# Kernel tuning notes

Measured on AMD Instinct MI355X. Metric: run time of the kernel, lower is better.

The kernel has to match this reference:

```python
import jax, jax.numpy as jnp
import numpy as np

B = 2
L = 1024
D_MODEL = 1024
D_INNER = 2048   # expand * d_model
D_STATE = 16
DT_RANK = 64     # ceil(d_model / 16)
D_CONV = 4


def setup_inputs() -> dict:
    key = jax.random.key(0)
    ks = jax.random.split(key, 8)
    def nrm(k, shape, scale):
        return jax.random.normal(k, shape, dtype=jnp.float32) * scale
    A_log = jnp.log(jnp.tile(jnp.arange(1, D_STATE + 1, dtype=jnp.float32)[None, :], (D_INNER, 1)))
    return dict(
        hidden_states=jax.random.normal(ks[0], (B, L, D_MODEL), dtype=jnp.float32),
        Win=nrm(ks[1], (D_MODEL, 2 * D_INNER), D_MODEL ** -0.5),
        Wx=nrm(ks[2], (D_INNER, DT_RANK + 2 * D_STATE), D_INNER ** -0.5),
        Wdt=nrm(ks[3], (DT_RANK, D_INNER), DT_RANK ** -0.5),
        dt_bias=nrm(ks[4], (D_INNER,), 1.0),
        Wout=nrm(ks[5], (D_INNER, D_MODEL), D_INNER ** -0.5),
        dw_kernel=nrm(ks[6], (D_CONV, D_INNER), 0.2),
        dw_bias=jnp.zeros((D_INNER,), dtype=jnp.float32),
        A_log=A_log,
        Dskip=jnp.ones((D_INNER,), dtype=jnp.float32),
    )


def _causal_depthwise_conv(x, kernel, bias):
    # x: (B, L, D_INNER), kernel: (k, D_INNER); dilation 1, causal left pad
    k = kernel.shape[0]
    Lq = x.shape[1]
    xpad = jnp.pad(x, ((0, 0), (k - 1, 0), (0, 0)))
    y = sum(xpad[:, i:i + Lq, :] * kernel[i] for i in range(k)) + bias
    return jax.nn.silu(y)


def _selective_scan(u, delta, A, Bm, Cm, Dskip, z):
    # u, delta, z: (B, L, D); A: (D, N); Bm, Cm: (B, L, N)
    deltaA = jnp.exp(jnp.einsum('bld,dn->bldn', delta, A))      # (B,L,D,N)
    deltaBu = jnp.einsum('bld,bln,bld->bldn', delta, Bm, u)     # (B,L,D,N)

    def step(x_prev, elems):
        dA, dBu, c = elems                                      # (B,D,N),(B,D,N),(B,N)
        x_new = dA * x_prev + dBu
        y = jnp.einsum('bdn,bn->bd', x_new, c)
        return x_new, y

    x0 = jnp.zeros((u.shape[0], u.shape[2], A.shape[1]), dtype=jnp.float32)
    _, ys = jax.lax.scan(
        step, x0,
        (deltaA.transpose(1, 0, 2, 3), deltaBu.transpose(1, 0, 2, 3), Cm.transpose(1, 0, 2)))
    y = ys.transpose(1, 0, 2) + u * Dskip                        # skip connection
    return y * jax.nn.silu(z)


def reference(hidden_states, Win, Wx, Wdt, dt_bias, Wout, dw_kernel, dw_bias, A_log, Dskip):
    xz = hidden_states @ Win                                     # (B,L,2*D_INNER)
    x, z = jnp.split(xz, 2, axis=-1)
    A = -jnp.exp(A_log)                                          # (D_INNER, D_STATE)
    x = _causal_depthwise_conv(x, dw_kernel, dw_bias)
    x_dbl = x @ Wx                                               # (B,L,DT_RANK+2*N)
    dt, Bm, Cm = jnp.split(x_dbl, [DT_RANK, DT_RANK + D_STATE], axis=-1)
    delta = jax.nn.softplus(dt @ Wdt + dt_bias)                  # delta_bias + softplus
    y = _selective_scan(x, delta, A, Bm, Cm, Dskip, z)
    return y @ Wout
```

## Files before the change

kernel.cpp:

```cpp
#include <hip/hip_runtime.h>
#include <hip/hip_bf16.h>
#include <math.h>

#define B_SZ 2
#define L_SZ 1024
#define DM 1024
#define DI 2048
#define NS 16
#define DTR 64
#define NCHUNK 16
#define CLEN 64
#define XDLD 128
#define KSPLIT 8

typedef unsigned short ushortT;
typedef __attribute__((ext_vector_type(8))) short short8;
typedef __attribute__((ext_vector_type(4))) float floatx4;

__device__ __forceinline__ ushortT f2bf(float f) {
  unsigned u = __float_as_uint(f);
  unsigned r = (u + 0x7fff + ((u >> 16) & 1)) >> 16;
  return (ushortT)r;
}

__device__ __forceinline__ float bf2f(ushortT v) {
  return __uint_as_float((unsigned)v << 16);
}

__device__ __forceinline__ float fexp2(float x) {
  float r;
  asm("v_exp_f32 %0, %1" : "=v"(r) : "v"(x));
  return r;
}

__device__ __forceinline__ void gl2lds16(const void* g, void* l) {
  __builtin_amdgcn_global_load_lds(
      (const __attribute__((address_space(1))) unsigned int*)g,
      (__attribute__((address_space(3))) unsigned int*)l, 16, 0, 0);
}

__device__ __forceinline__ unsigned stash_addr(unsigned i) {
  return (i >> 10) * 4096 + 1024 + (i & 1023);
}

__device__ __forceinline__ void tr_body(const float* __restrict__ src,
                                        ushortT* __restrict__ dst, int R, int C,
                                        int bx, int by, int tx, int ty,
                                        float (*t)[33]) {
#pragma unroll
  for (int j = 0; j < 4; ++j)
    t[ty + j * 8][tx] = src[(size_t)(by + ty + j * 8) * C + bx + tx];
  __syncthreads();
#pragma unroll
  for (int j = 0; j < 4; ++j)
    dst[(size_t)(bx + ty + j * 8) * R + by + tx] = f2bf(t[tx][ty + j * 8]);
}

__global__ __launch_bounds__(256) void prep_all(
    const float* __restrict__ hidden, ushortT* __restrict__ hidb,
    const float* __restrict__ Win, ushortT* __restrict__ WinT,
    const float* __restrict__ Wx, ushortT* __restrict__ WxT,
    const float* __restrict__ Wdt, ushortT* __restrict__ WdtT,
    const float* __restrict__ Wout, ushortT* __restrict__ WoutT) {
  __shared__ float t[32][33];
  const int blk = blockIdx.x;
  const int tid = threadIdx.x;
  const int tx = tid & 31, ty = tid >> 5;
  if (blk < 2048) {
    const int i = blk * 256 + tid;
    float4 v = ((const float4*)hidden)[i];
    unsigned lo = (unsigned)f2bf(v.x) | ((unsigned)f2bf(v.y) << 16);
    unsigned hi = (unsigned)f2bf(v.z) | ((unsigned)f2bf(v.w) << 16);
    ((uint2*)hidb)[i] = make_uint2(lo, hi);
  } else if (blk < 6144) {
    const int rel = blk - 2048;
    tr_body(Win, WinT, DM, 2 * DI, (rel & 127) * 32, (rel >> 7) * 32, tx, ty, t);
  } else if (blk < 7168) {
    const int rel = blk - 6144;
    const int k = (rel & 7) * 256 + tid;
    const int n = rel >> 3;
    WxT[(size_t)n * DI + k] = (n < 96) ? f2bf(Wx[(size_t)k * 96 + n]) : (ushortT)0;
  } else if (blk < 7296) {
    const int rel = blk - 7168;
    tr_body(Wdt, WdtT, DTR, DI, (rel & 63) * 32, (rel >> 6) * 32, tx, ty, t);
  } else {
    const int rel = blk - 7296;
    tr_body(Wout, WoutT, DI, DM, (rel & 31) * 32, (rel >> 5) * 32, tx, ty, t);
  }
}

__global__ __launch_bounds__(512) void gemm1_big(
    const ushortT* __restrict__ A, int lda,
    const ushortT* __restrict__ BT, int ldb,
    float* __restrict__ C, int ldc, int K) {
  __shared__ __align__(16) char smem[128 * 128 + 128 * 128];
  char* As = smem;
  char* Bs = smem + 128 * 128;
  const int tid = threadIdx.x;
  const int lane = tid & 63;
  const int quad = lane >> 4;
  const int l16 = lane & 15;
  const int wid = tid >> 6;
  const int wm = wid & 1;
  const int wn = wid >> 1;
  const int m0 = blockIdx.y * 128;
  const int n0 = blockIdx.x * 128;

  floatx4 acc[4][2] = {};

  for (int k0 = 0; k0 < K; k0 += 64) {
    for (int i = tid; i < 128 * 8; i += 512) {
      const int r = i >> 3, c = i & 7;
      const int cg = c ^ (r & 7);
      gl2lds16(A + (size_t)(m0 + r) * lda + k0 + cg * 8, As + (i - lane) * 16);
    }
    for (int i = tid; i < 128 * 8; i += 512) {
      const int r = i >> 3, c = i & 7;
      const int cg = c ^ (r & 7);
      gl2lds16(BT + (size_t)(n0 + r) * ldb + k0 + cg * 8, Bs + (i - lane) * 16);
    }
    __syncthreads();

    short8 afr[4][2], bfr[2][2];
#pragma unroll
    for (int i = 0; i < 4; ++i) {
      const int r = wm * 64 + i * 16 + l16;
#pragma unroll
      for (int s = 0; s < 2; ++s)
        afr[i][s] = *(const short8*)(As + r * 128 + (((s * 4 + quad) ^ (r & 7)) * 16));
    }
#pragma unroll
    for (int j = 0; j < 2; ++j) {
      const int r = wn * 32 + j * 16 + l16;
#pragma unroll
      for (int s = 0; s < 2; ++s)
        bfr[j][s] = *(const short8*)(Bs + r * 128 + (((s * 4 + quad) ^ (r & 7)) * 16));
    }
#pragma unroll
    for (int s = 0; s < 2; ++s)
#pragma unroll
      for (int i = 0; i < 4; ++i)
#pragma unroll
        for (int j = 0; j < 2; ++j)
          acc[i][j] = __builtin_amdgcn_mfma_f32_16x16x32_bf16(afr[i][s], bfr[j][s],
                                                              acc[i][j], 0, 0, 0);
    __syncthreads();
  }
#pragma unroll
  for (int i = 0; i < 4; ++i)
#pragma unroll
    for (int j = 0; j < 2; ++j)
#pragma unroll
      for (int r = 0; r < 4; ++r) {
        const int m = m0 + wm * 64 + i * 16 + quad * 4 + r;
        const int n = n0 + wn * 32 + j * 16 + l16;
        C[(size_t)m * ldc + n] = acc[i][j][r];
      }
}

__global__ __launch_bounds__(256) void gemm_out(
    const ushortT* __restrict__ A, int lda,
    const ushortT* __restrict__ BT, int ldb,
    float* __restrict__ C) {
  __shared__ __align__(16) char smem[64 * 128 + 64 * 128];
  char* As = smem;
  char* Bs = smem + 64 * 128;
  const int tid = threadIdx.x;
  const int lane = tid & 63;
  const int quad = lane >> 4;
  const int l16 = lane & 15;
  const int wid = tid >> 6;
  const int wm = wid & 1;
  const int wn = wid >> 1;
  const int m0 = blockIdx.y * 64;
  const int n0 = blockIdx.x * 64;

  floatx4 acc[2][2] = {};

  for (int k0 = 0; k0 < DI; k0 += 64) {
    for (int i = tid; i < 64 * 8; i += 256) {
      const int r = i >> 3, c = i & 7;
      const int cg = c ^ (r & 7);
      gl2lds16(A + (size_t)(m0 + r) * lda + k0 + cg * 8, As + (i - lane) * 16);
    }
    for (int i = tid; i < 64 * 8; i += 256) {
      const int r = i >> 3, c = i & 7;
      const int cg = c ^ (r & 7);
      gl2lds16(BT + (size_t)(n0 + r) * ldb + k0 + cg * 8, Bs + (i - lane) * 16);
    }
    __syncthreads();

    short8 afr[2][2], bfr[2][2];
#pragma unroll
    for (int i = 0; i < 2; ++i) {
      const int m = wm * 32 + i * 16 + l16;
#pragma unroll
      for (int s = 0; s < 2; ++s)
        afr[i][s] = *(const short8*)(As + m * 128 + (((s * 4 + quad) ^ (m & 7)) * 16));
    }
#pragma unroll
    for (int j = 0; j < 2; ++j) {
      const int n = wn * 32 + j * 16 + l16;
#pragma unroll
      for (int s = 0; s < 2; ++s)
        bfr[j][s] = *(const short8*)(Bs + n * 128 + (((s * 4 + quad) ^ (n & 7)) * 16));
    }
#pragma unroll
    for (int s = 0; s < 2; ++s)
#pragma unroll
      for (int i = 0; i < 2; ++i)
#pragma unroll
        for (int j = 0; j < 2; ++j)
          acc[i][j] = __builtin_amdgcn_mfma_f32_16x16x32_bf16(afr[i][s], bfr[j][s],
                                                              acc[i][j], 0, 0, 0);
    __syncthreads();
  }
#pragma unroll
  for (int i = 0; i < 2; ++i)
#pragma unroll
    for (int j = 0; j < 2; ++j)
#pragma unroll
      for (int r = 0; r < 4; ++r) {
        const int m = m0 + wm * 32 + i * 16 + quad * 4 + r;
        const int n = n0 + wn * 32 + j * 16 + l16;
        C[(size_t)m * DM + n] = acc[i][j][r];
      }
}

__global__ __launch_bounds__(256) void gemm_xdbl_mfma(
    const ushortT* __restrict__ xcb, const ushortT* __restrict__ WxT,
    float* __restrict__ part) {
  __shared__ __align__(16) char smem[64 * 64 + 128 * 64];
  char* As = smem;
  char* Bs = smem + 64 * 64;
  const int tid = threadIdx.x;
  const int lane = tid & 63;
  const int quad = lane >> 4;
  const int l16 = lane & 15;
  const int wid = tid >> 6;
  const int wm = wid & 1;
  const int wn = wid >> 1;
  const int m0 = blockIdx.x * 64;
  const int kbase = blockIdx.y * (DI / KSPLIT);

  floatx4 acc[2][4] = {};

  for (int kk = 0; kk < DI / KSPLIT; kk += 32) {
    const int k0 = kbase + kk;
    for (int i = tid; i < 64 * 4; i += 256) {
      const int r = i >> 2, c = i & 3;
      const int cg = c ^ (r & 3);
      gl2lds16(xcb + (size_t)(m0 + r) * DI + k0 + cg * 8, As + (i - lane) * 16);
    }
    for (int i = tid; i < 128 * 4; i += 256) {
      const int r = i >> 2, c = i & 3;
      const int cg = c ^ (r & 3);
      gl2lds16(WxT + (size_t)r * DI + k0 + cg * 8, Bs + (i - lane) * 16);
    }
    __syncthreads();

    short8 afr[2], bfr[4];
#pragma unroll
    for (int i = 0; i < 2; ++i) {
      const int m = wm * 32 + i * 16 + l16;
      afr[i] = *(const short8*)(As + m * 64 + ((quad ^ (m & 3)) * 16));
    }
#pragma unroll
    for (int j = 0; j < 4; ++j) {
      const int n = wn * 64 + j * 16 + l16;
      bfr[j] = *(const short8*)(Bs + n * 64 + ((quad ^ (n & 3)) * 16));
    }
#pragma unroll
    for (int i = 0; i < 2; ++i)
#pragma unroll
      for (int j = 0; j < 4; ++j)
        acc[i][j] = __builtin_amdgcn_mfma_f32_16x16x32_bf16(afr[i], bfr[j],
                                                            acc[i][j], 0, 0, 0);
    __syncthreads();
  }
  float* out = part + (size_t)blockIdx.y * (B_SZ * L_SZ * XDLD);
#pragma unroll
  for (int i = 0; i < 2; ++i)
#pragma unroll
    for (int j = 0; j < 4; ++j)
#pragma unroll
      for (int r = 0; r < 4; ++r) {
        const int m = m0 + wm * 32 + i * 16 + quad * 4 + r;
        const int n = wn * 64 + j * 16 + l16;
        out[(size_t)m * XDLD + n] = acc[i][j][r];
      }
}

__global__ __launch_bounds__(256) void xdbl_reduce(const float* __restrict__ part,
                                                   float* __restrict__ xdbl,
                                                   ushortT* __restrict__ dtb) {
  const int i = blockIdx.x * 256 + threadIdx.x;
  float4 a = ((const float4*)part)[i];
#pragma unroll
  for (int s = 1; s < KSPLIT; ++s) {
    const float4 b = ((const float4*)part)[(size_t)s * (B_SZ * L_SZ * XDLD / 4) + i];
    a.x += b.x; a.y += b.y; a.z += b.z; a.w += b.w;
  }
  ((float4*)xdbl)[i] = a;
  const int row = i >> 5;
  const int c4 = (i & 31) * 4;
  if (c4 < DTR) {
    const unsigned lo = (unsigned)f2bf(a.x) | ((unsigned)f2bf(a.y) << 16);
    const unsigned hi = (unsigned)f2bf(a.z) | ((unsigned)f2bf(a.w) << 16);
    ((uint2*)dtb)[row * (DTR / 4) + (c4 >> 2)] = make_uint2(lo, hi);
  }
}

__global__ __launch_bounds__(256) void conv_silu(
    const float* __restrict__ xz, const float* __restrict__ kern,
    const float* __restrict__ bias, ushortT* __restrict__ xcb) {
  const int d = blockIdx.y * 256 + threadIdx.x;
  const int b = blockIdx.x >> 7;
  const int l0 = (blockIdx.x & 127) * 8;
  const int row0 = b * L_SZ + l0;
  const float k0v = kern[0 * DI + d], k1v = kern[1 * DI + d];
  const float k2v = kern[2 * DI + d], k3v = kern[3 * DI + d];
  float xv[11];
#pragma unroll
  for (int i = 0; i < 11; ++i) {
    const int l = l0 - 3 + i;
    xv[i] = (l >= 0) ? xz[((size_t)(b * L_SZ + l)) * 4096 + d] : 0.f;
  }
  const float bs = bias[d];
#pragma unroll
  for (int j = 0; j < 8; ++j) {
    float a = bs;
    a = fmaf(xv[j], k0v, a);
    a = fmaf(xv[j + 1], k1v, a);
    a = fmaf(xv[j + 2], k2v, a);
    a = fmaf(xv[j + 3], k3v, a);
    xcb[(size_t)(row0 + j) * DI + d] = f2bf(a / (1.f + __expf(-a)));
  }
}

__global__ __launch_bounds__(256) void gemm_delta_mfma(
    const ushortT* __restrict__ dtb, const ushortT* __restrict__ WdtT,
    const float* __restrict__ dt_bias, float* __restrict__ delta) {
  __shared__ __align__(16) char smem[64 * 128 + 64 * 128];
  char* As = smem;
  char* Bs = smem + 64 * 128;
  const int tid = threadIdx.x;
  const int lane = tid & 63;
  const int quad = lane >> 4;
  const int l16 = lane & 15;
  const int wid = tid >> 6;
  const int wm = wid & 1;
  const int wn = wid >> 1;
  const int m0 = blockIdx.x * 64;
  const int n0 = blockIdx.y * 64;

  for (int i = tid; i < 64 * 8; i += 256) {
    const int r = i >> 3, c = i & 7;
    const int cg = c ^ (r & 7);
    gl2lds16(dtb + (size_t)(m0 + r) * DTR + cg * 8, As + (i - lane) * 16);
  }
  for (int i = tid; i < 64 * 8; i += 256) {
    const int r = i >> 3, c = i & 7;
    const int cg = c ^ (r & 7);
    gl2lds16(WdtT + (size_t)(n0 + r) * DTR + cg * 8, Bs + (i - lane) * 16);
  }
  __syncthreads();

  floatx4 acc[2][2] = {};
  short8 afr[2][2], bfr[2][2];
#pragma unroll
  for (int i = 0; i < 2; ++i) {
    const int m = wm * 32 + i * 16 + l16;
#pragma unroll
    for (int s = 0; s < 2; ++s)
      afr[i][s] = *(const short8*)(As + m * 128 + (((s * 4 + quad) ^ (m & 7)) * 16));
  }
#pragma unroll
  for (int j = 0; j < 2; ++j) {
    const int n = wn * 32 + j * 16 + l16;
#pragma unroll
    for (int s = 0; s < 2; ++s)
      bfr[j][s] = *(const short8*)(Bs + n * 128 + (((s * 4 + quad) ^ (n & 7)) * 16));
  }
#pragma unroll
  for (int s = 0; s < 2; ++s)
#pragma unroll
    for (int i = 0; i < 2; ++i)
#pragma unroll
      for (int j = 0; j < 2; ++j)
        acc[i][j] = __builtin_amdgcn_mfma_f32_16x16x32_bf16(afr[i][s], bfr[j][s],
                                                            acc[i][j], 0, 0, 0);

#pragma unroll
  for (int i = 0; i < 2; ++i)
#pragma unroll
    for (int j = 0; j < 2; ++j) {
      const int n = n0 + wn * 32 + j * 16 + l16;
      const float bias = dt_bias[n];
#pragma unroll
      for (int r = 0; r < 4; ++r) {
        const int m = m0 + wm * 32 + i * 16 + quad * 4 + r;
        const float a = acc[i][j][r] + bias;
        delta[(size_t)m * DI + n] = (a > 20.f) ? a : __logf(1.f + __expf(a));
      }
    }
}

__global__ __launch_bounds__(256) void scan_phase1(
    const float* __restrict__ delta, const ushortT* __restrict__ xcb,
    const float* __restrict__ xdbl, const float* __restrict__ A_log,
    float* __restrict__ xz) {
  const int bx = blockIdx.x;
  const int b = bx >> 10;
  const int c = (bx >> 6) & 15;
  const int dt = bx & 63;
  const int tid = threadIdx.x;
  const int dl = tid >> 3, nq = tid & 7;
  const int d = dt * 32 + dl;
  const int row0 = b * L_SZ + c * CLEN;

  __shared__ float Bsh[CLEN][16];
  for (int i = tid; i < CLEN * 16; i += 256)
    Bsh[i >> 4][i & 15] = xdbl[(size_t)(row0 + (i >> 4)) * XDLD + 64 + (i & 15)];

  float Av2[2];
#pragma unroll
  for (int j = 0; j < 2; ++j)
    Av2[j] = -__expf(A_log[d * 16 + nq * 2 + j]) * 1.44269504f;

  const float* dp = delta + (size_t)row0 * DI + d;
  const ushortT* up = xcb + (size_t)row0 * DI + d;

  float dB[8], uB[8];
#pragma unroll
  for (int j = 0; j < 8; ++j) {
    dB[j] = dp[(size_t)j * DI];
    uB[j] = bf2f(up[(size_t)j * DI]);
  }
  float x0 = 0.f, x1 = 0.f, sd = 0.f;
  __syncthreads();

#pragma unroll 1
  for (int g = 0; g < 8; ++g) {
    float dN[8] = {}, uN[8] = {};
    if (g + 1 < 8) {
      const int nr = (g + 1) * 8;
#pragma unroll
      for (int j = 0; j < 8; ++j) {
        dN[j] = dp[(size_t)(nr + j) * DI];
        uN[j] = bf2f(up[(size_t)(nr + j) * DI]);
      }
    }
#pragma unroll
    for (int j = 0; j < 8; ++j) {
      const float dlt = dB[j];
      const float2 Bv = *(const float2*)&Bsh[g * 8 + j][nq * 2];
      sd += dlt;
      const float t = dlt * uB[j];
      x0 = fmaf(fexp2(dlt * Av2[0]), x0, t * Bv.x);
      x1 = fmaf(fexp2(dlt * Av2[1]), x1, t * Bv.y);
    }
#pragma unroll
    for (int j = 0; j < 8; ++j) { dB[j] = dN[j]; uB[j] = uN[j]; }
  }
  const unsigned e = ((unsigned)((b * NCHUNK + c) * DI + d)) * 16 + nq * 2;
  *(float2*)&xz[stash_addr(e)] = make_float2(fexp2(Av2[0] * sd), fexp2(Av2[1] * sd));
  *(float2*)&xz[stash_addr((1u << 20) + e)] = make_float2(x0, x1);
}

__global__ __launch_bounds__(256) void scan_phase3(
    const float* __restrict__ delta, const ushortT* __restrict__ xcb,
    const float* __restrict__ xdbl, const float* __restrict__ A_log,
    const float* __restrict__ Dskip, float* __restrict__ xz) {
  const int bx = blockIdx.x;
  const int b = bx >> 10;
  const int c = (bx >> 6) & 15;
  const int dt = bx & 63;
  const int tid = threadIdx.x;
  const int dl = tid >> 3, nq = tid & 7;
  const int d = dt * 32 + dl;
  const int row0 = b * L_SZ + c * CLEN;

  __shared__ float Bsh[CLEN][16], Csh[CLEN][16];
  for (int i = tid; i < CLEN * 32; i += 256) {
    const int r = i >> 5, q = i & 31;
    const float v = xdbl[(size_t)(row0 + r) * XDLD + 64 + q];
    if (q < 16) Bsh[r][q] = v; else Csh[r][q - 16] = v;
  }

  float Av2[2];
#pragma unroll
  for (int j = 0; j < 2; ++j)
    Av2[j] = -__expf(A_log[d * 16 + nq * 2 + j]) * 1.44269504f;
  const float Dsk = Dskip[d];

  float x0 = 0.f, x1 = 0.f;
  for (int cc = 0; cc < c; ++cc) {
    const unsigned e = ((unsigned)((b * NCHUNK + cc) * DI + d)) * 16 + nq * 2;
    const float2 P = *(const float2*)&xz[stash_addr(e)];
    const float2 S = *(const float2*)&xz[stash_addr((1u << 20) + e)];
    x0 = fmaf(P.x, x0, S.x);
    x1 = fmaf(P.y, x1, S.y);
  }
  __syncthreads();

  const float* dp = delta + (size_t)row0 * DI + d;
  const ushortT* up = xcb + (size_t)row0 * DI + d;
  const float* zp = xz + (size_t)row0 * 4096 + DI + d;
  ushortT* yb = (ushortT*)xz;

  float dB[8], uB[8];
#pragma unroll
  for (int j = 0; j < 8; ++j) {
    dB[j] = dp[(size_t)j * DI];
    uB[j] = bf2f(up[(size_t)j * DI]);
  }
  float zB = zp[(size_t)nq * 4096];

#pragma unroll 1
  for (int g = 0; g < 8; ++g) {
    float dN[8] = {}, uN[8] = {}, zN = 0.f;
    if (g + 1 < 8) {
      const int nr = (g + 1) * 8;
#pragma unroll
      for (int j = 0; j < 8; ++j) {
        dN[j] = dp[(size_t)(nr + j) * DI];
        uN[j] = bf2f(up[(size_t)(nr + j) * DI]);
      }
      zN = zp[(size_t)(nr + nq) * 4096];
    }
    float yk = 0.f, uk = 0.f;
#pragma unroll
    for (int j = 0; j < 8; ++j) {
      const float dlt = dB[j];
      const float u = uB[j];
      const float2 Bv = *(const float2*)&Bsh[g * 8 + j][nq * 2];
      const float2 Cv = *(const float2*)&Csh[g * 8 + j][nq * 2];
      const float t = dlt * u;
      x0 = fmaf(fexp2(dlt * Av2[0]), x0, t * Bv.x);
      x1 = fmaf(fexp2(dlt * Av2[1]), x1, t * Bv.y);
      float y = fmaf(x1, Cv.y, x0 * Cv.x);
      y += __shfl_xor(y, 1);
      y += __shfl_xor(y, 2);
      y += __shfl_xor(y, 4);
      if (nq == j) { yk = y; uk = u; }
    }
    const float sig = zB / (1.f + __expf(-zB));
    yb[(size_t)(row0 + g * 8 + nq) * 8192 + d] = f2bf(fmaf(uk, Dsk, yk) * sig);
#pragma unroll
    for (int j = 0; j < 8; ++j) { dB[j] = dN[j]; uB[j] = uN[j]; }
    zB = zN;
  }
}

extern "C" void kernel_launch(void* const* d_in, const int* in_sizes, int n_in,
                              void* d_out, int out_size, void* d_ws, size_t ws_size,
                              hipStream_t stream) {
  const float* hidden  = (const float*)d_in[0];
  const float* Win     = (const float*)d_in[1];
  const float* Wx      = (const float*)d_in[2];
  const float* Wdt     = (const float*)d_in[3];
  const float* dt_bias = (const float*)d_in[4];
  const float* Wout    = (const float*)d_in[5];
  const float* dwk     = (const float*)d_in[6];
  const float* dwb     = (const float*)d_in[7];
  const float* A_log   = (const float*)d_in[8];
  const float* Dskip   = (const float*)d_in[9];

  char* ws = (char*)d_ws;
  float* xz       = (float*)ws;
  float* shared16 = (float*)(ws + (32u << 20));
  ushortT* xcb    = (ushortT*)(ws + (48u << 20));
  ushortT* WoutT  = (ushortT*)(ws + (56u << 20));
  char* dob = (char*)d_out;
  ushortT* hidb = (ushortT*)dob;
  float* xdbl   = (float*)(dob + (4u << 20));
  ushortT* WxT  = (ushortT*)(dob + (5u << 20));
  ushortT* WdtT = (ushortT*)(dob + (5u << 20) + (512u << 10));
  ushortT* dtb  = (ushortT*)(dob + (5u << 20) + (768u << 10));

  prep_all<<<dim3(9344), 256, 0, stream>>>(hidden, hidb, Win, (ushortT*)shared16,
                                           Wx, WxT, Wdt, WdtT, Wout, WoutT);
  gemm1_big<<<dim3(4096 / 128, 2048 / 128), 512, 0, stream>>>(
      hidb, DM, (ushortT*)shared16, DM, xz, 2 * DI, DM);
  conv_silu<<<dim3(B_SZ * L_SZ / 8, DI / 256), 256, 0, stream>>>(xz, dwk, dwb, xcb);
  gemm_xdbl_mfma<<<dim3(B_SZ * L_SZ / 64, KSPLIT), 256, 0, stream>>>(
      xcb, WxT, shared16);
  xdbl_reduce<<<dim3(B_SZ * L_SZ * XDLD / 1024), 256, 0, stream>>>(shared16, xdbl, dtb);
  gemm_delta_mfma<<<dim3(B_SZ * L_SZ / 64, DI / 64), 256, 0, stream>>>(
      dtb, WdtT, dt_bias, shared16);
  scan_phase1<<<dim3(2048), 256, 0, stream>>>(
      shared16, xcb, xdbl, A_log, xz);
  scan_phase3<<<dim3(2048), 256, 0, stream>>>(
      shared16, xcb, xdbl, A_log, Dskip, xz);
  gemm_out<<<dim3(DM / 64, 2048 / 64), 256, 0, stream>>>(
      (ushortT*)xz, 4 * DI, WoutT, DI, (float*)d_out);
}
```

Before: 226.8 us.

## Remap scan threads to own 8 states each, two threads per channel

Both scan kernels now assign two threads per channel, each holding 8 of the 16 state elements, instead of eight threads per channel holding 2 states each. This cuts the y reduction to a single shuffle, makes every thread compute the z gate and output rather than one selected lane, and vectorizes the shared-memory and stash accesses to float4. The grid shrinks from 2048 to 512 blocks of 256 threads. The trade-off is more registers per thread and fewer total waves for hiding latency, while each channel's delta/u/z values are now loaded by 2 threads instead of 8.

```diff
diff --git a/kernel.cpp b/kernel.cpp
--- a/kernel.cpp
+++ b/kernel.cpp
@@ -411,22 +411,31 @@
     const float* __restrict__ xdbl, const float* __restrict__ A_log,
     float* __restrict__ xz) {
   const int bx = blockIdx.x;
-  const int b = bx >> 10;
-  const int c = (bx >> 6) & 15;
-  const int dt = bx & 63;
+  const int b = bx >> 8;
+  const int c = (bx >> 4) & 15;
+  const int dblk = bx & 15;
   const int tid = threadIdx.x;
-  const int dl = tid >> 3, nq = tid & 7;
-  const int d = dt * 32 + dl;
+  const int half = tid & 1;
+  const int d = dblk * 128 + (tid >> 1);
   const int row0 = b * L_SZ + c * CLEN;
 
   __shared__ float Bsh[CLEN][16];
   for (int i = tid; i < CLEN * 16; i += 256)
     Bsh[i >> 4][i & 15] = xdbl[(size_t)(row0 + (i >> 4)) * XDLD + 64 + (i & 15)];
 
-  float Av2[2];
-#pragma unroll
-  for (int j = 0; j < 2; ++j)
-    Av2[j] = -__expf(A_log[d * 16 + nq * 2 + j]) * 1.44269504f;
+  float Av2[8];
+  {
+    const float4 a0 = *(const float4*)&A_log[d * 16 + half * 8];
+    const float4 a1 = *(const float4*)&A_log[d * 16 + half * 8 + 4];
+    Av2[0] = -__expf(a0.x) * 1.44269504f;
+    Av2[1] = -__expf(a0.y) * 1.44269504f;
+    Av2[2] = -__expf(a0.z) * 1.44269504f;
+    Av2[3] = -__expf(a0.w) * 1.44269504f;
+    Av2[4] = -__expf(a1.x) * 1.44269504f;
+    Av2[5] = -__expf(a1.y) * 1.44269504f;
+    Av2[6] = -__expf(a1.z) * 1.44269504f;
+    Av2[7] = -__expf(a1.w) * 1.44269504f;
+  }
 
   const float* dp = delta + (size_t)row0 * DI + d;
   const ushortT* up = xcb + (size_t)row0 * DI + d;
@@ -437,7 +446,8 @@
     dB[j] = dp[(size_t)j * DI];
     uB[j] = bf2f(up[(size_t)j * DI]);
   }
-  float x0 = 0.f, x1 = 0.f, sd = 0.f;
+  float x[8] = {};
+  float sd = 0.f;
   __syncthreads();
 
 #pragma unroll 1
@@ -454,18 +464,31 @@
 #pragma unroll
     for (int j = 0; j < 8; ++j) {
       const float dlt = dB[j];
-      const float2 Bv = *(const float2*)&Bsh[g * 8 + j][nq * 2];
+      const float t = dlt * uB[j];
+      const float4 B0 = *(const float4*)&Bsh[g * 8 + j][half * 8];
+      const float4 B1 = *(const float4*)&Bsh[g * 8 + j][half * 8 + 4];
       sd += dlt;
-      const float t = dlt * uB[j];
-      x0 = fmaf(fexp2(dlt * Av2[0]), x0, t * Bv.x);
-      x1 = fmaf(fexp2(dlt * Av2[1]), x1, t * Bv.y);
+      x[0] = fmaf(fexp2(dlt * Av2[0]), x[0], t * B0.x);
+      x[1] = fmaf(fexp2(dlt * Av2[1]), x[1], t * B0.y);
+      x[2] = fmaf(fexp2(dlt * Av2[2]), x[2], t * B0.z);
+      x[3] = fmaf(fexp2(dlt * Av2[3]), x[3], t * B0.w);
+      x[4] = fmaf(fexp2(dlt * Av2[4]), x[4], t * B1.x);
+      x[5] = fmaf(fexp2(dlt * Av2[5]), x[5], t * B1.y);
+      x[6] = fmaf(fexp2(dlt * Av2[6]), x[6], t * B1.z);
+      x[7] = fmaf(fexp2(dlt * Av2[7]), x[7], t * B1.w);
     }
 #pragma unroll
     for (int j = 0; j < 8; ++j) { dB[j] = dN[j]; uB[j] = uN[j]; }
   }
-  const unsigned e = ((unsigned)((b * NCHUNK + c) * DI + d)) * 16 + nq * 2;
-  *(float2*)&xz[stash_addr(e)] = make_float2(fexp2(Av2[0] * sd), fexp2(Av2[1] * sd));
-  *(float2*)&xz[stash_addr((1u << 20) + e)] = make_float2(x0, x1);
+  const unsigned e = ((unsigned)((b * NCHUNK + c) * DI + d)) * 16 + half * 8;
+  *(float4*)&xz[stash_addr(e)] =
+      make_float4(fexp2(Av2[0] * sd), fexp2(Av2[1] * sd),
+                  fexp2(Av2[2] * sd), fexp2(Av2[3] * sd));
+  *(float4*)&xz[stash_addr(e + 4)] =
+      make_float4(fexp2(Av2[4] * sd), fexp2(Av2[5] * sd),
+                  fexp2(Av2[6] * sd), fexp2(Av2[7] * sd));
+  *(float4*)&xz[stash_addr((1u << 20) + e)] = make_float4(x[0], x[1], x[2], x[3]);
+  *(float4*)&xz[stash_addr((1u << 20) + e + 4)] = make_float4(x[4], x[5], x[6], x[7]);
 }
 
 __global__ __launch_bounds__(256) void scan_phase3(
@@ -473,12 +496,12 @@
     const float* __restrict__ xdbl, const float* __restrict__ A_log,
     const float* __restrict__ Dskip, float* __restrict__ xz) {
   const int bx = blockIdx.x;
-  const int b = bx >> 10;
-  const int c = (bx >> 6) & 15;
-  const int dt = bx & 63;
+  const int b = bx >> 8;
+  const int c = (bx >> 4) & 15;
+  const int dblk = bx & 15;
   const int tid = threadIdx.x;
-  const int dl = tid >> 3, nq = tid & 7;
-  const int d = dt * 32 + dl;
+  const int half = tid & 1;
+  const int d = dblk * 128 + (tid >> 1);
   const int row0 = b * L_SZ + c * CLEN;
 
   __shared__ float Bsh[CLEN][16], Csh[CLEN][16];
@@ -488,19 +511,36 @@
     if (q < 16) Bsh[r][q] = v; else Csh[r][q - 16] = v;
   }
 
-  float Av2[2];
-#pragma unroll
-  for (int j = 0; j < 2; ++j)
-    Av2[j] = -__expf(A_log[d * 16 + nq * 2 + j]) * 1.44269504f;
+  float Av2[8];
+  {
+    const float4 a0 = *(const float4*)&A_log[d * 16 + half * 8];
+    const float4 a1 = *(const float4*)&A_log[d * 16 + half * 8 + 4];
+    Av2[0] = -__expf(a0.x) * 1.44269504f;
+    Av2[1] = -__expf(a0.y) * 1.44269504f;
+    Av2[2] = -__expf(a0.z) * 1.44269504f;
+    Av2[3] = -__expf(a0.w) * 1.44269504f;
+    Av2[4] = -__expf(a1.x) * 1.44269504f;
+    Av2[5] = -__expf(a1.y) * 1.44269504f;
+    Av2[6] = -__expf(a1.z) * 1.44269504f;
+    Av2[7] = -__expf(a1.w) * 1.44269504f;
+  }
   const float Dsk = Dskip[d];
 
-  float x0 = 0.f, x1 = 0.f;
+  float x[8] = {};
   for (int cc = 0; cc < c; ++cc) {
-    const unsigned e = ((unsigned)((b * NCHUNK + cc) * DI + d)) * 16 + nq * 2;
-    const float2 P = *(const float2*)&xz[stash_addr(e)];
-    const float2 S = *(const float2*)&xz[stash_addr((1u << 20) + e)];
-    x0 = fmaf(P.x, x0, S.x);
-    x1 = fmaf(P.y, x1, S.y);
+    const unsigned e = ((unsigned)((b * NCHUNK + cc) * DI + d)) * 16 + half * 8;
+    const float4 P0 = *(const float4*)&xz[stash_addr(e)];
+    const float4 P1 = *(const float4*)&xz[stash_addr(e + 4)];
+    const float4 S0 = *(const float4*)&xz[stash_addr((1u << 20) + e)];
+    const float4 S1 = *(const float4*)&xz[stash_addr((1u << 20) + e + 4)];
+    x[0] = fmaf(P0.x, x[0], S0.x);
+    x[1] = fmaf(P0.y, x[1], S0.y);
+    x[2] = fmaf(P0.z, x[2], S0.z);
+    x[3] = fmaf(P0.w, x[3], S0.w);
+    x[4] = fmaf(P1.x, x[4], S1.x);
+    x[5] = fmaf(P1.y, x[5], S1.y);
+    x[6] = fmaf(P1.z, x[6], S1.z);
+    x[7] = fmaf(P1.w, x[7], S1.w);
   }
   __syncthreads();
 
@@ -509,47 +549,59 @@
   const float* zp = xz + (size_t)row0 * 4096 + DI + d;
   ushortT* yb = (ushortT*)xz;
 
-  float dB[8], uB[8];
+  float dB[8], uB[8], zB[8];
 #pragma unroll
   for (int j = 0; j < 8; ++j) {
     dB[j] = dp[(size_t)j * DI];
     uB[j] = bf2f(up[(size_t)j * DI]);
-  }
-  float zB = zp[(size_t)nq * 4096];
+    zB[j] = zp[(size_t)j * 4096];
+  }
 
 #pragma unroll 1
   for (int g = 0; g < 8; ++g) {
-    float dN[8] = {}, uN[8] = {}, zN = 0.f;
+    float dN[8] = {}, uN[8] = {}, zN[8] = {};
     if (g + 1 < 8) {
       const int nr = (g + 1) * 8;
 #pragma unroll
       for (int j = 0; j < 8; ++j) {
         dN[j] = dp[(size_t)(nr + j) * DI];
         uN[j] = bf2f(up[(size_t)(nr + j) * DI]);
+        zN[j] = zp[(size_t)(nr + j) * 4096];
       }
-      zN = zp[(size_t)(nr + nq) * 4096];
-    }
-    float yk = 0.f, uk = 0.f;
+    }
 #pragma unroll
     for (int j = 0; j < 8; ++j) {
       const float dlt = dB[j];
       const float u = uB[j];
-      const float2 Bv = *(const float2*)&Bsh[g * 8 + j][nq * 2];
-      const float2 Cv = *(const float2*)&Csh[g * 8 + j][nq * 2];
       const float t = dlt * u;
-      x0 = fmaf(fexp2(dlt * Av2[0]), x0, t * Bv.x);
-      x1 = fmaf(fexp2(dlt * Av2[1]), x1, t * Bv.y);
-      float y = fmaf(x1, Cv.y, x0 * Cv.x);
+      const float4 B0 = *(const float4*)&Bsh[g * 8 + j][half * 8];
+      const float4 B1 = *(const float4*)&Bsh[g * 8 + j][half * 8 + 4];
+      const float4 C0 = *(const float4*)&Csh[g * 8 + j][half * 8];
+      const float4 C1 = *(const float4*)&Csh[g * 8 + j][half * 8 + 4];
+      x[0] = fmaf(fexp2(dlt * Av2[0]), x[0], t * B0.x);
+      x[1] = fmaf(fexp2(dlt * Av2[1]), x[1], t * B0.y);
+      x[2] = fmaf(fexp2(dlt * Av2[2]), x[2], t * B0.z);
+      x[3] = fmaf(fexp2(dlt * Av2[3]), x[3], t * B0.w);
+      x[4] = fmaf(fexp2(dlt * Av2[4]), x[4], t * B1.x);
+      x[5] = fmaf(fexp2(dlt * Av2[5]), x[5], t * B1.y);
+      x[6] = fmaf(fexp2(dlt * Av2[6]), x[6], t * B1.z);
+      x[7] = fmaf(fexp2(dlt * Av2[7]), x[7], t * B1.w);
+      float y = x[0] * C0.x;
+      y = fmaf(x[1], C0.y, y);
+      y = fmaf(x[2], C0.z, y);
+      y = fmaf(x[3], C0.w, y);
+      y = fmaf(x[4], C1.x, y);
+      y = fmaf(x[5], C1.y, y);
+      y = fmaf(x[6], C1.z, y);
+      y = fmaf(x[7], C1.w, y);
       y += __shfl_xor(y, 1);
-      y += __shfl_xor(y, 2);
-      y += __shfl_xor(y, 4);
-      if (nq == j) { yk = y; uk = u; }
-    }
-    const float sig = zB / (1.f + __expf(-zB));
-    yb[(size_t)(row0 + g * 8 + nq) * 8192 + d] = f2bf(fmaf(uk, Dsk, yk) * sig);
-#pragma unroll
-    for (int j = 0; j < 8; ++j) { dB[j] = dN[j]; uB[j] = uN[j]; }
-    zB = zN;
+      const float z = zB[j];
+      const float sig = z / (1.f + __expf(-z));
+      const float gv = fmaf(u, Dsk, y) * sig;
+      if (!half) yb[(size_t)(row0 + g * 8 + j) * 8192 + d] = f2bf(gv);
+    }
+#pragma unroll
+    for (int j = 0; j < 8; ++j) { dB[j] = dN[j]; uB[j] = uN[j]; zB[j] = zN[j]; }
   }
 }
 
@@ -589,9 +641,9 @@
   xdbl_reduce<<<dim3(B_SZ * L_SZ * XDLD / 1024), 256, 0, stream>>>(shared16, xdbl, dtb);
   gemm_delta_mfma<<<dim3(B_SZ * L_SZ / 64, DI / 64), 256, 0, stream>>>(
       dtb, WdtT, dt_bias, shared16);
-  scan_phase1<<<dim3(2048), 256, 0, stream>>>(
+  scan_phase1<<<dim3(512), 256, 0, stream>>>(
       shared16, xcb, xdbl, A_log, xz);
-  scan_phase3<<<dim3(2048), 256, 0, stream>>>(
+  scan_phase3<<<dim3(512), 256, 0, stream>>>(
       shared16, xcb, xdbl, A_log, Dskip, xz);
   gemm_out<<<dim3(DM / 64, 2048 / 64), 256, 0, stream>>>(
       (ushortT*)xz, 4 * DI, WoutT, DI, (float*)d_out);
```

Result: no change. 224.6 us (-1.0%).
